# Kernel optimization log

Measured on AMD Instinct MI355X. Metric: run time of the kernel, lower is better.

Reference implementation:

```python
import jax, jax.numpy as jnp
import numpy as np
from jax import lax

DIM = 512
HEADS = 8
SPLIT = 7  # split_size; idx=0 -> H_sp=H, W_sp=SPLIT


def setup_inputs() -> dict:
    key = jax.random.key(0)
    k1, k2 = jax.random.split(key, 2)
    B, H, W = 16, 56, 56
    qkv = jax.random.normal(k1, (3, B, H * W, DIM), dtype=jnp.float32)
    conv_w = jax.random.normal(k2, (DIM, 1, 3, 3), dtype=jnp.float32) * 0.05  # depthwise 3x3
    conv_b = jnp.zeros((DIM,), dtype=jnp.float32)
    return {"qkv": qkv, "conv_w": conv_w, "conv_b": conv_b, "H": H, "W": W}


def _lepe_attn(qkv, conv_w, conv_b, H, W):
    q, k, v = qkv[0], qkv[1], qkv[2]
    B, L, C = q.shape
    hd = C // HEADS
    scale = hd ** -0.5
    H_sp, W_sp = H, SPLIT  # idx == 0 (horizontal stripes)
    S = H_sp * W_sp
    nWh, nWw = H // H_sp, W // W_sp

    def to_win_heads(x):
        # [B, L, C] -> [B*nW, heads, S, hd]
        x = x.reshape(B, nWh, H_sp, nWw, W_sp, C)
        x = x.transpose(0, 1, 3, 2, 4, 5).reshape(-1, S, HEADS, hd)
        return x.transpose(0, 2, 1, 3)

    qw = to_win_heads(q)
    kw = to_win_heads(k)

    # v as per-window images [B*nW, C, H_sp, W_sp] for depthwise-conv LePE
    vimg = v.reshape(B, nWh, H_sp, nWw, W_sp, C)
    vimg = vimg.transpose(0, 1, 3, 5, 2, 4).reshape(-1, C, H_sp, W_sp)
    lepe = lax.conv_general_dilated(
        vimg, conv_w, window_strides=(1, 1), padding=[(1, 1), (1, 1)],
        dimension_numbers=("NCHW", "OIHW", "NCHW"), feature_group_count=C,
    ) + conv_b[None, :, None, None]
    lepe = lepe.reshape(-1, HEADS, hd, S).transpose(0, 1, 3, 2)  # [B*nW, heads, S, hd]
    vw = vimg.reshape(-1, HEADS, hd, S).transpose(0, 1, 3, 2)

    attn = jnp.einsum("whsd,whtd->whst", qw * scale, kw)
    attn = jax.nn.softmax(attn, axis=-1)
    out = jnp.einsum("whst,whtd->whsd", attn, vw) + lepe

    # windows -> image: [B*nW, heads, S, hd] -> [B, L, C]
    out = out.transpose(0, 2, 1, 3).reshape(-1, S, C)
    out = out.reshape(B, nWh, nWw, H_sp, W_sp, C)
    out = out.transpose(0, 1, 3, 2, 4, 5).reshape(B, L, C)
    return out


def reference(qkv, conv_w, conv_b, H, W):
    return _lepe_attn(qkv, conv_w, conv_b, H, W)
```

## Files before the change

### kernel.cpp

```cpp
#include <hip/hip_runtime.h>

#define B_    16
#define HIMG  56
#define WIMG  56
#define L_    3136
#define C_    512
#define NH_   8
#define HD_   64
#define S_    392
#define NKT   13
#define NQT   13

typedef short short4v __attribute__((ext_vector_type(4)));
typedef short short8  __attribute__((ext_vector_type(8)));
typedef float f32x4   __attribute__((ext_vector_type(4)));
typedef float f32x16  __attribute__((ext_vector_type(16)));

__device__ __forceinline__ short f2bf(float f) {
    union { float f; unsigned int i; } x; x.f = f;
    unsigned int i = x.i;
    i += 0x7fffu + ((i >> 16) & 1u);
    return (short)(i >> 16);
}
__device__ __forceinline__ int l_of(int s, int ww) {
    int h = s / 7;
    int wp = s - h * 7;
    return h * WIMG + ww * 7 + wp;
}

__global__ __launch_bounds__(256) void lepe_kernel(
    const float* __restrict__ vp, const float* __restrict__ cw,
    const float* __restrict__ cb, float* __restrict__ out)
{
    __shared__ __align__(16) float sW[9 * 516];

    for (int i = threadIdx.x; i < 1152; i += 256) {
        f32x4 v = *(const f32x4*)(cw + i * 4);
#pragma unroll
        for (int j = 0; j < 4; ++j) {
            int e = 4 * i + j;
            int c = e / 9;
            int k = e - 9 * c;
            sW[k * 516 + c] = v[j];
        }
    }
    __syncthreads();

    int g    = blockIdx.x * 256 + threadIdx.x;
    int c0   = (g & 127) * 4;
    int rest = g >> 7;
    int l    = rest % L_;
    int h    = l / WIMG;
    int wim  = l - h * WIMG;
    int wsp  = wim % 7;

    f32x4 acc = *(const f32x4*)(cb + c0);
    const long long base = (long long)rest * C_ + c0;
#pragma unroll
    for (int dh = -1; dh <= 1; ++dh) {
        int hh = h + dh;
        if (hh < 0 || hh >= HIMG) continue;
#pragma unroll
        for (int dw = -1; dw <= 1; ++dw) {
            int wp2 = wsp + dw;
            if (wp2 < 0 || wp2 >= 7) continue;
            f32x4 vv = *(const f32x4*)(vp + base + (long long)(dh * WIMG + dw) * C_);
            int k = (dh + 1) * 3 + (dw + 1);
            f32x4 wv = *(const f32x4*)&sW[k * 516 + c0];
#pragma unroll
            for (int i = 0; i < 4; ++i) acc[i] += vv[i] * wv[i];
        }
    }
    *(f32x4*)(out + base) = acc;
}

__global__ __launch_bounds__(512) void attn_kernel(
    const float* __restrict__ qkv, float* __restrict__ out)
{
    const int head = blockIdx.x;
    const int win  = blockIdx.y;
    const int b    = win >> 3;
    const int ww   = win & 7;

    const int tid  = threadIdx.x;
    const int wave = tid >> 6;
    const int lane = tid & 63;
    const int l31  = lane & 31;
    const int hi   = lane >> 5;

    const float* kp = qkv + (long long)B_ * L_ * C_;
    const float* vp = qkv + 2LL * (long long)B_ * L_ * C_;

    __shared__ __align__(16) short sAll[56896];
    short* sK = sAll;
    short* sV = sAll + 28224;

    const int st_r = tid >> 4;
    const int st_c = (tid & 15) * 4;

    const long long kvbase = (long long)b * L_ * C_ + head * HD_;

#pragma unroll
    for (int p = 0; p < 13; ++p) {
        int t = p * 32 + st_r;
        if (t < S_) {
            f32x4 kv = *(const f32x4*)(kp + kvbase + (long long)l_of(t, ww) * C_ + st_c);
            short4v ks;
#pragma unroll
            for (int j = 0; j < 4; ++j) ks[j] = f2bf(kv[j]);
            *(short4v*)&sK[t * 72 + st_c] = ks;
        }
    }
#pragma unroll
    for (int p = 0; p < 14; ++p) {
        int t = p * 32 + st_r;
        f32x4 vv = {0.f, 0.f, 0.f, 0.f};
        if (t < S_)
            vv = *(const f32x4*)(vp + kvbase + (long long)l_of(t, ww) * C_ + st_c);
#pragma unroll
        for (int j = 0; j < 4; ++j) {
            int d  = st_c + j;
            int sw = ((d >> 3) & 3) << 4;
            sV[d * 448 + (t ^ sw)] = f2bf(vv[j]);
        }
    }
    __syncthreads();

    const float SCL = 0.125f * 1.44269504088896340736f;

    for (int qt = wave; qt < NQT; qt += 8) {
        const int qrow0 = qt * 32;
        int qs = qrow0 + l31; if (qs > S_ - 1) qs = S_ - 1;
        const float* qp = qkv + (long long)b * L_ * C_
                        + (long long)l_of(qs, ww) * C_ + head * HD_ + hi * 8;
        short8 bq[4];
#pragma unroll
        for (int kk = 0; kk < 4; ++kk) {
            f32x4 x0 = *(const f32x4*)(qp + kk * 16);
            f32x4 x1 = *(const f32x4*)(qp + kk * 16 + 4);
            short8 t;
#pragma unroll
            for (int j = 0; j < 4; ++j) { t[j] = f2bf(x0[j]); t[4 + j] = f2bf(x1[j]); }
            bq[kk] = t;
        }

        f32x16 Oa0, Oa1;
#pragma unroll
        for (int r = 0; r < 16; ++r) { Oa0[r] = 0.f; Oa1[r] = 0.f; }
        float mrun = -1e30f, lrun = 0.f;

        for (int ch = 0; ch < NKT; ++ch) {
            const int kt0 = ch * 32;
            int krow = kt0 + l31; if (krow > S_ - 1) krow = S_ - 1;
            const short* kr = &sK[krow * 72 + hi * 8];

            f32x16 acc;
#pragma unroll
            for (int r = 0; r < 16; ++r) acc[r] = 0.f;
#pragma unroll
            for (int kk = 0; kk < 4; ++kk) {
                short8 ak = *(const short8*)(kr + kk * 16);
                acc = __builtin_amdgcn_mfma_f32_32x32x16_bf16(ak, bq[kk], acc, 0, 0, 0);
            }
            float pm = -1e30f;
#pragma unroll
            for (int r = 0; r < 16; ++r) {
                int key = kt0 + (r & 3) + 8 * (r >> 2) + 4 * hi;
                float v = acc[r] * SCL;
                v = (key < S_) ? v : -1e30f;
                acc[r] = v;
                pm = fmaxf(pm, v);
            }
            pm = fmaxf(pm, __shfl_xor(pm, 32));
            if (__any(pm > mrun + 8.f)) {
                float mnew  = fmaxf(mrun, pm);
                float alpha = exp2f(mrun - mnew);
#pragma unroll
                for (int r = 0; r < 16; ++r) { Oa0[r] *= alpha; Oa1[r] *= alpha; }
                lrun *= alpha;
                mrun = mnew;
            }
            float rs = 0.f;
#pragma unroll
            for (int r = 0; r < 16; ++r) {
                float p = exp2f(acc[r] - mrun);
                acc[r] = p;
                rs += p;
            }
            rs += __shfl_xor(rs, 32);
            lrun += rs;
            unsigned int u[8];
#pragma unroll
            for (int a = 0; a < 4; ++a)
#pragma unroll
                for (int h = 0; h < 2; ++h) {
                    unsigned int r_;
                    asm("v_cvt_pk_bf16_f32 %0, %1, %2"
                        : "=v"(r_) : "v"(acc[4 * a + 2 * h]), "v"(acc[4 * a + 2 * h + 1]));
                    u[a * 2 + h] = r_;
                }
#pragma unroll
            for (int kkp = 0; kkp < 2; ++kkp) {
                unsigned int sA0 = (unsigned int)__shfl_xor((int)u[4 * kkp + 0], 32);
                unsigned int sA1 = (unsigned int)__shfl_xor((int)u[4 * kkp + 1], 32);
                unsigned int sB0 = (unsigned int)__shfl_xor((int)u[4 * kkp + 2], 32);
                unsigned int sB1 = (unsigned int)__shfl_xor((int)u[4 * kkp + 3], 32);
                union { unsigned int w[4]; short8 s; } pb;
                pb.w[0] = hi ? sB0 : u[4 * kkp + 0];
                pb.w[1] = hi ? sB1 : u[4 * kkp + 1];
                pb.w[2] = hi ? u[4 * kkp + 2] : sA0;
                pb.w[3] = hi ? u[4 * kkp + 3] : sA1;
                const int Tb = kt0 + kkp * 16 + hi * 8;
                {
                    int d = l31;
                    short8 av = *(const short8*)&sV[d * 448 + (Tb ^ (((d >> 3) & 3) << 4))];
                    Oa0 = __builtin_amdgcn_mfma_f32_32x32x16_bf16(av, pb.s, Oa0, 0, 0, 0);
                }
                {
                    int d = 32 + l31;
                    short8 av = *(const short8*)&sV[d * 448 + (Tb ^ (((d >> 3) & 3) << 4))];
                    Oa1 = __builtin_amdgcn_mfma_f32_32x32x16_bf16(av, pb.s, Oa1, 0, 0, 0);
                }
            }
        }

        if (qrow0 + l31 < S_) {
            float inv = 1.0f / lrun;
            float* op = out + (long long)b * L_ * C_
                      + (long long)l_of(qrow0 + l31, ww) * C_ + head * HD_;
#pragma unroll
            for (int g = 0; g < 4; ++g) {
                float* p4 = op + g * 8 + hi * 4;
                f32x4 t = *(f32x4*)p4;
#pragma unroll
                for (int j = 0; j < 4; ++j) t[j] += Oa0[4 * g + j] * inv;
                *(f32x4*)p4 = t;
            }
#pragma unroll
            for (int g = 0; g < 4; ++g) {
                float* p4 = op + 32 + g * 8 + hi * 4;
                f32x4 t = *(f32x4*)p4;
#pragma unroll
                for (int j = 0; j < 4; ++j) t[j] += Oa1[4 * g + j] * inv;
                *(f32x4*)p4 = t;
            }
        }
    }
}

extern "C" void kernel_launch(void* const* d_in, const int* in_sizes, int n_in,
                              void* d_out, int out_size, void* d_ws, size_t ws_size,
                              hipStream_t stream) {
    (void)in_sizes; (void)n_in; (void)d_ws; (void)ws_size; (void)out_size;
    const float* qkv = (const float*)d_in[0];
    const float* cw  = (const float*)d_in[1];
    const float* cb  = (const float*)d_in[2];
    float* out = (float*)d_out;
    const float* vp = qkv + 2LL * (long long)B_ * L_ * C_;

    lepe_kernel<<<dim3((B_ * L_ * (C_ / 4)) / 256), dim3(256), 0, stream>>>(vp, cw, cb, out);
    attn_kernel<<<dim3(NH_, B_ * 8), dim3(512), 0, stream>>>(qkv, out);
}
```

Baseline: 588.3 us.

## Make attention kernel persistent and prefetch next item's K into registers

The attention kernel now launches 256 workgroups, each processing four (window, head) items in sequence instead of one block per item. While it computes the current item, it prefetches the next item's K tile into registers, and it loads V into registers before the barrier, so global loads can overlap with compute. The costs are higher register pressure from the kbuf/vbuf arrays (27 float4 per thread) and extra barriers. With one block per CU, occupancy and latency hiding may drop.

```diff
diff --git a/kernel.cpp b/kernel.cpp
--- a/kernel.cpp
+++ b/kernel.cpp
@@ -10,6 +10,7 @@
 #define S_    392
 #define NKT   13
 #define NQT   13
+#define NITEM 4
 
 typedef short short4v __attribute__((ext_vector_type(4)));
 typedef short short8  __attribute__((ext_vector_type(8)));
@@ -77,11 +78,7 @@
 __global__ __launch_bounds__(512) void attn_kernel(
     const float* __restrict__ qkv, float* __restrict__ out)
 {
-    const int head = blockIdx.x;
-    const int win  = blockIdx.y;
-    const int b    = win >> 3;
-    const int ww   = win & 7;
-
+    const int wg   = blockIdx.x;
     const int tid  = threadIdx.x;
     const int wave = tid >> 6;
     const int lane = tid & 63;
@@ -98,151 +95,197 @@
     const int st_r = tid >> 4;
     const int st_c = (tid & 15) * 4;
 
-    const long long kvbase = (long long)b * L_ * C_ + head * HD_;
-
-#pragma unroll
-    for (int p = 0; p < 13; ++p) {
-        int t = p * 32 + st_r;
-        if (t < S_) {
-            f32x4 kv = *(const f32x4*)(kp + kvbase + (long long)l_of(t, ww) * C_ + st_c);
-            short4v ks;
-#pragma unroll
-            for (int j = 0; j < 4; ++j) ks[j] = f2bf(kv[j]);
-            *(short4v*)&sK[t * 72 + st_c] = ks;
+    f32x4 kbuf[13];
+    f32x4 vbuf[14];
+
+    {
+        const int id = wg;
+        const int head0 = id & 7, win0 = id >> 3;
+        const int b0 = win0 >> 3, ww0 = win0 & 7;
+        const long long kvb = (long long)b0 * L_ * C_ + head0 * HD_;
+#pragma unroll
+        for (int p = 0; p < 13; ++p) {
+            int t = p * 32 + st_r;
+            if (t < S_)
+                kbuf[p] = *(const f32x4*)(kp + kvb + (long long)l_of(t, ww0) * C_ + st_c);
         }
     }
-#pragma unroll
-    for (int p = 0; p < 14; ++p) {
-        int t = p * 32 + st_r;
-        f32x4 vv = {0.f, 0.f, 0.f, 0.f};
-        if (t < S_)
-            vv = *(const f32x4*)(vp + kvbase + (long long)l_of(t, ww) * C_ + st_c);
-#pragma unroll
-        for (int j = 0; j < 4; ++j) {
-            int d  = st_c + j;
-            int sw = ((d >> 3) & 3) << 4;
-            sV[d * 448 + (t ^ sw)] = f2bf(vv[j]);
-        }
-    }
-    __syncthreads();
+    __builtin_amdgcn_sched_barrier(0);
 
     const float SCL = 0.125f * 1.44269504088896340736f;
 
-    for (int qt = wave; qt < NQT; qt += 8) {
-        const int qrow0 = qt * 32;
-        int qs = qrow0 + l31; if (qs > S_ - 1) qs = S_ - 1;
-        const float* qp = qkv + (long long)b * L_ * C_
-                        + (long long)l_of(qs, ww) * C_ + head * HD_ + hi * 8;
-        short8 bq[4];
-#pragma unroll
-        for (int kk = 0; kk < 4; ++kk) {
-            f32x4 x0 = *(const f32x4*)(qp + kk * 16);
-            f32x4 x1 = *(const f32x4*)(qp + kk * 16 + 4);
-            short8 t;
-#pragma unroll
-            for (int j = 0; j < 4; ++j) { t[j] = f2bf(x0[j]); t[4 + j] = f2bf(x1[j]); }
-            bq[kk] = t;
-        }
-
-        f32x16 Oa0, Oa1;
-#pragma unroll
-        for (int r = 0; r < 16; ++r) { Oa0[r] = 0.f; Oa1[r] = 0.f; }
-        float mrun = -1e30f, lrun = 0.f;
-
-        for (int ch = 0; ch < NKT; ++ch) {
-            const int kt0 = ch * 32;
-            int krow = kt0 + l31; if (krow > S_ - 1) krow = S_ - 1;
-            const short* kr = &sK[krow * 72 + hi * 8];
-
-            f32x16 acc;
-#pragma unroll
-            for (int r = 0; r < 16; ++r) acc[r] = 0.f;
+    for (int item = 0; item < NITEM; ++item) {
+        const int id   = item * 256 + wg;
+        const int head = id & 7;
+        const int win  = id >> 3;
+        const int b    = win >> 3;
+        const int ww   = win & 7;
+        const long long kvbase = (long long)b * L_ * C_ + head * HD_;
+
+#pragma unroll
+        for (int p = 0; p < 14; ++p) {
+            int t = p * 32 + st_r;
+            f32x4 vv = {0.f, 0.f, 0.f, 0.f};
+            if (t < S_)
+                vv = *(const f32x4*)(vp + kvbase + (long long)l_of(t, ww) * C_ + st_c);
+            vbuf[p] = vv;
+        }
+        __builtin_amdgcn_sched_barrier(0);
+
+        __syncthreads();
+
+#pragma unroll
+        for (int p = 0; p < 13; ++p) {
+            int t = p * 32 + st_r;
+            if (t < S_) {
+                short4v ks;
+#pragma unroll
+                for (int j = 0; j < 4; ++j) ks[j] = f2bf(kbuf[p][j]);
+                *(short4v*)&sK[t * 72 + st_c] = ks;
+            }
+        }
+#pragma unroll
+        for (int p = 0; p < 14; ++p) {
+            int t = p * 32 + st_r;
+#pragma unroll
+            for (int j = 0; j < 4; ++j) {
+                int d  = st_c + j;
+                int sw = ((d >> 3) & 3) << 4;
+                sV[d * 448 + (t ^ sw)] = f2bf(vbuf[p][j]);
+            }
+        }
+        __syncthreads();
+
+        if (item < NITEM - 1) {
+            const int id2 = (item + 1) * 256 + wg;
+            const int head2 = id2 & 7, win2 = id2 >> 3;
+            const int b2 = win2 >> 3, ww2 = win2 & 7;
+            const long long kvb2 = (long long)b2 * L_ * C_ + head2 * HD_;
+#pragma unroll
+            for (int p = 0; p < 13; ++p) {
+                int t = p * 32 + st_r;
+                if (t < S_)
+                    kbuf[p] = *(const f32x4*)(kp + kvb2 + (long long)l_of(t, ww2) * C_ + st_c);
+            }
+            __builtin_amdgcn_sched_barrier(0);
+        }
+
+        for (int qt = wave; qt < NQT; qt += 8) {
+            const int qrow0 = qt * 32;
+            int qs = qrow0 + l31; if (qs > S_ - 1) qs = S_ - 1;
+            const float* qp = qkv + (long long)b * L_ * C_
+                            + (long long)l_of(qs, ww) * C_ + head * HD_ + hi * 8;
+            short8 bq[4];
 #pragma unroll
             for (int kk = 0; kk < 4; ++kk) {
-                short8 ak = *(const short8*)(kr + kk * 16);
-                acc = __builtin_amdgcn_mfma_f32_32x32x16_bf16(ak, bq[kk], acc, 0, 0, 0);
-            }
-            float pm = -1e30f;
-#pragma unroll
-            for (int r = 0; r < 16; ++r) {
-                int key = kt0 + (r & 3) + 8 * (r >> 2) + 4 * hi;
-                float v = acc[r] * SCL;
-                v = (key < S_) ? v : -1e30f;
-                acc[r] = v;
-                pm = fmaxf(pm, v);
-            }
-            pm = fmaxf(pm, __shfl_xor(pm, 32));
-            if (__any(pm > mrun + 8.f)) {
-                float mnew  = fmaxf(mrun, pm);
-                float alpha = exp2f(mrun - mnew);
-#pragma unroll
-                for (int r = 0; r < 16; ++r) { Oa0[r] *= alpha; Oa1[r] *= alpha; }
-                lrun *= alpha;
-                mrun = mnew;
-            }
-            float rs = 0.f;
-#pragma unroll
-            for (int r = 0; r < 16; ++r) {
-                float p = exp2f(acc[r] - mrun);
-                acc[r] = p;
-                rs += p;
-            }
-            rs += __shfl_xor(rs, 32);
-            lrun += rs;
-            unsigned int u[8];
-#pragma unroll
-            for (int a = 0; a < 4; ++a)
-#pragma unroll
-                for (int h = 0; h < 2; ++h) {
-                    unsigned int r_;
-                    asm("v_cvt_pk_bf16_f32 %0, %1, %2"
-                        : "=v"(r_) : "v"(acc[4 * a + 2 * h]), "v"(acc[4 * a + 2 * h + 1]));
-                    u[a * 2 + h] = r_;
-                }
-#pragma unroll
-            for (int kkp = 0; kkp < 2; ++kkp) {
-                unsigned int sA0 = (unsigned int)__shfl_xor((int)u[4 * kkp + 0], 32);
-                unsigned int sA1 = (unsigned int)__shfl_xor((int)u[4 * kkp + 1], 32);
-                unsigned int sB0 = (unsigned int)__shfl_xor((int)u[4 * kkp + 2], 32);
-                unsigned int sB1 = (unsigned int)__shfl_xor((int)u[4 * kkp + 3], 32);
-                union { unsigned int w[4]; short8 s; } pb;
-                pb.w[0] = hi ? sB0 : u[4 * kkp + 0];
-                pb.w[1] = hi ? sB1 : u[4 * kkp + 1];
-                pb.w[2] = hi ? u[4 * kkp + 2] : sA0;
-                pb.w[3] = hi ? u[4 * kkp + 3] : sA1;
-                const int Tb = kt0 + kkp * 16 + hi * 8;
-                {
-                    int d = l31;
-                    short8 av = *(const short8*)&sV[d * 448 + (Tb ^ (((d >> 3) & 3) << 4))];
-                    Oa0 = __builtin_amdgcn_mfma_f32_32x32x16_bf16(av, pb.s, Oa0, 0, 0, 0);
-                }
-                {
-                    int d = 32 + l31;
-                    short8 av = *(const short8*)&sV[d * 448 + (Tb ^ (((d >> 3) & 3) << 4))];
-                    Oa1 = __builtin_amdgcn_mfma_f32_32x32x16_bf16(av, pb.s, Oa1, 0, 0, 0);
-                }
-            }
-        }
-
-        if (qrow0 + l31 < S_) {
-            float inv = 1.0f / lrun;
-            float* op = out + (long long)b * L_ * C_
-                      + (long long)l_of(qrow0 + l31, ww) * C_ + head * HD_;
-#pragma unroll
-            for (int g = 0; g < 4; ++g) {
-                float* p4 = op + g * 8 + hi * 4;
-                f32x4 t = *(f32x4*)p4;
-#pragma unroll
-                for (int j = 0; j < 4; ++j) t[j] += Oa0[4 * g + j] * inv;
-                *(f32x4*)p4 = t;
-            }
-#pragma unroll
-            for (int g = 0; g < 4; ++g) {
-                float* p4 = op + 32 + g * 8 + hi * 4;
-                f32x4 t = *(f32x4*)p4;
-#pragma unroll
-                for (int j = 0; j < 4; ++j) t[j] += Oa1[4 * g + j] * inv;
-                *(f32x4*)p4 = t;
+                f32x4 x0 = *(const f32x4*)(qp + kk * 16);
+                f32x4 x1 = *(const f32x4*)(qp + kk * 16 + 4);
+                short8 t;
+#pragma unroll
+                for (int j = 0; j < 4; ++j) { t[j] = f2bf(x0[j]); t[4 + j] = f2bf(x1[j]); }
+                bq[kk] = t;
+            }
+
+            f32x16 Oa0, Oa1;
+#pragma unroll
+            for (int r = 0; r < 16; ++r) { Oa0[r] = 0.f; Oa1[r] = 0.f; }
+            float mrun = -1e30f, lrun = 0.f;
+
+            for (int ch = 0; ch < NKT; ++ch) {
+                const int kt0 = ch * 32;
+                int krow = kt0 + l31; if (krow > S_ - 1) krow = S_ - 1;
+                const short* kr = &sK[krow * 72 + hi * 8];
+
+                f32x16 acc;
+#pragma unroll
+                for (int r = 0; r < 16; ++r) acc[r] = 0.f;
+#pragma unroll
+                for (int kk = 0; kk < 4; ++kk) {
+                    short8 ak = *(const short8*)(kr + kk * 16);
+                    acc = __builtin_amdgcn_mfma_f32_32x32x16_bf16(ak, bq[kk], acc, 0, 0, 0);
+                }
+                float pm = -1e30f;
+#pragma unroll
+                for (int r = 0; r < 16; ++r) {
+                    int key = kt0 + (r & 3) + 8 * (r >> 2) + 4 * hi;
+                    float v = acc[r] * SCL;
+                    v = (key < S_) ? v : -1e30f;
+                    acc[r] = v;
+                    pm = fmaxf(pm, v);
+                }
+                pm = fmaxf(pm, __shfl_xor(pm, 32));
+                if (__any(pm > mrun + 8.f)) {
+                    float mnew  = fmaxf(mrun, pm);
+                    float alpha = exp2f(mrun - mnew);
+#pragma unroll
+                    for (int r = 0; r < 16; ++r) { Oa0[r] *= alpha; Oa1[r] *= alpha; }
+                    lrun *= alpha;
+                    mrun = mnew;
+                }
+                float rs = 0.f;
+#pragma unroll
+                for (int r = 0; r < 16; ++r) {
+                    float p = exp2f(acc[r] - mrun);
+                    acc[r] = p;
+                    rs += p;
+                }
+                rs += __shfl_xor(rs, 32);
+                lrun += rs;
+                unsigned int u[8];
+#pragma unroll
+                for (int a = 0; a < 4; ++a)
+#pragma unroll
+                    for (int h = 0; h < 2; ++h) {
+                        unsigned int r_;
+                        asm("v_cvt_pk_bf16_f32 %0, %1, %2"
+                            : "=v"(r_) : "v"(acc[4 * a + 2 * h]), "v"(acc[4 * a + 2 * h + 1]));
+                        u[a * 2 + h] = r_;
+                    }
+#pragma unroll
+                for (int kkp = 0; kkp < 2; ++kkp) {
+                    unsigned int sA0 = (unsigned int)__shfl_xor((int)u[4 * kkp + 0], 32);
+                    unsigned int sA1 = (unsigned int)__shfl_xor((int)u[4 * kkp + 1], 32);
+                    unsigned int sB0 = (unsigned int)__shfl_xor((int)u[4 * kkp + 2], 32);
+                    unsigned int sB1 = (unsigned int)__shfl_xor((int)u[4 * kkp + 3], 32);
+                    union { unsigned int w[4]; short8 s; } pb;
+                    pb.w[0] = hi ? sB0 : u[4 * kkp + 0];
+                    pb.w[1] = hi ? sB1 : u[4 * kkp + 1];
+                    pb.w[2] = hi ? u[4 * kkp + 2] : sA0;
+                    pb.w[3] = hi ? u[4 * kkp + 3] : sA1;
+                    const int Tb = kt0 + kkp * 16 + hi * 8;
+                    {
+                        int d = l31;
+                        short8 av = *(const short8*)&sV[d * 448 + (Tb ^ (((d >> 3) & 3) << 4))];
+                        Oa0 = __builtin_amdgcn_mfma_f32_32x32x16_bf16(av, pb.s, Oa0, 0, 0, 0);
+                    }
+                    {
+                        int d = 32 + l31;
+                        short8 av = *(const short8*)&sV[d * 448 + (Tb ^ (((d >> 3) & 3) << 4))];
+                        Oa1 = __builtin_amdgcn_mfma_f32_32x32x16_bf16(av, pb.s, Oa1, 0, 0, 0);
+                    }
+                }
+            }
+
+            if (qrow0 + l31 < S_) {
+                float inv = 1.0f / lrun;
+                float* op = out + (long long)b * L_ * C_
+                          + (long long)l_of(qrow0 + l31, ww) * C_ + head * HD_;
+#pragma unroll
+                for (int g = 0; g < 4; ++g) {
+                    float* p4 = op + g * 8 + hi * 4;
+                    f32x4 t = *(f32x4*)p4;
+#pragma unroll
+                    for (int j = 0; j < 4; ++j) t[j] += Oa0[4 * g + j] * inv;
+                    *(f32x4*)p4 = t;
+                }
+#pragma unroll
+                for (int g = 0; g < 4; ++g) {
+                    float* p4 = op + 32 + g * 8 + hi * 4;
+                    f32x4 t = *(f32x4*)p4;
+#pragma unroll
+                    for (int j = 0; j < 4; ++j) t[j] += Oa1[4 * g + j] * inv;
+                    *(f32x4*)p4 = t;
+                }
             }
         }
     }
@@ -259,5 +302,5 @@
     const float* vp = qkv + 2LL * (long long)B_ * L_ * C_;
 
     lepe_kernel<<<dim3((B_ * L_ * (C_ / 4)) / 256), dim3(256), 0, stream>>>(vp, cw, cb, out);
-    attn_kernel<<<dim3(NH_, B_ * 8), dim3(512), 0, stream>>>(qkv, out);
-}
+    attn_kernel<<<dim3(256), dim3(512), 0, stream>>>(qkv, out);
+}
```

Result: no change. 586.8 us (-0.3%).
